# Kernel optimization log

Measured on AMD Instinct MI355X. Metric: run time of the kernel, lower is better.

Reference implementation:

```python
import jax, jax.numpy as jnp
import numpy as np

NUM_EMBEDDINGS = 4096
EMBEDDING_DIM = 512
N_TOKENS = 32768
COMMITMENT_COST = 0.25


def setup_inputs() -> dict:
    key = jax.random.key(0)
    k1, k2 = jax.random.split(key)
    flat_input = jax.random.normal(k1, (N_TOKENS, EMBEDDING_DIM), dtype=jnp.float32)
    # torch init: uniform(-1/K, 1/K)
    weight = jax.random.uniform(k2, (NUM_EMBEDDINGS, EMBEDDING_DIM), dtype=jnp.float32,
                                minval=-1.0 / NUM_EMBEDDINGS, maxval=1.0 / NUM_EMBEDDINGS)
    return {"flat_input": flat_input, "weight": weight}


def reference(flat_input, weight):
    distances = (jnp.sum(flat_input ** 2, axis=1, keepdims=True)
                 + jnp.sum(weight ** 2, axis=1)
                 - 2.0 * jnp.matmul(flat_input, weight.T))
    encoding_indices = jnp.argmin(distances, axis=1)  # [N]
    # one-hot @ weight == direct gather of codebook rows
    quantized = weight[encoding_indices]  # [N, D]

    e_latent_loss = jnp.mean((jax.lax.stop_gradient(quantized) - flat_input) ** 2, axis=1)
    q_latent_loss = jnp.mean((quantized - jax.lax.stop_gradient(flat_input)) ** 2, axis=1)
    loss = q_latent_loss + COMMITMENT_COST * e_latent_loss  # [N]

    # straight-through estimator
    quantized_st = flat_input + jax.lax.stop_gradient(quantized - flat_input)

    # avg_probs = mean of one-hot encodings over batch = normalized code counts
    counts = jnp.zeros((NUM_EMBEDDINGS,), dtype=flat_input.dtype).at[encoding_indices].add(1.0)
    avg_probs = counts / flat_input.shape[0]
    perplexity = jnp.exp(-jnp.sum(avg_probs * jnp.log(avg_probs + 1e-10)))

    return quantized_st, loss, perplexity, encoding_indices
```

## Files before the change

### kernel.cpp

```cpp
#include <hip/hip_runtime.h>
#include <math.h>

#define N_TOK 32768
#define K_CODES 4096
#define DIM 512
#define COMMIT 0.25f
#define NCAND 8
#define NSPLIT 2
#define SPLIT_CODES (K_CODES / NSPLIT)
#define NITER (SPLIT_CODES / 256)
#define BIAS 0.125f

typedef short s16x8 __attribute__((ext_vector_type(8)));
typedef float f32x4 __attribute__((ext_vector_type(4)));
typedef unsigned int uint32;
typedef unsigned long long u64;
typedef unsigned short u16;

__device__ __forceinline__ u16 f2bf(float f) {
    uint32 b = __float_as_uint(f);
    return (u16)((b + 0x7FFFu + ((b >> 16) & 1u)) >> 16);
}

__device__ __forceinline__ void gload16(const u16* g, u16* l) {
    __builtin_amdgcn_global_load_lds(
        (const __attribute__((address_space(1))) void*)g,
        (__attribute__((address_space(3))) void*)l,
        16, 0, 0);
}

__global__ __launch_bounds__(256) void tobf16_kernel(const float* __restrict__ src,
                                                     u16* __restrict__ dst, int n4) {
    int i = blockIdx.x * 256 + threadIdx.x;
    int stride = gridDim.x * 256;
    for (; i < n4; i += stride) {
        float4 v = ((const float4*)src)[i];
        ushort4 o;
        o.x = f2bf(v.x); o.y = f2bf(v.y); o.z = f2bf(v.z); o.w = f2bf(v.w);
        ((ushort4*)dst)[i] = o;
    }
}

__global__ __launch_bounds__(256) void rowsq_np_kernel(const float* __restrict__ a,
                                                       float* __restrict__ out,
                                                       int nrows) {
    #pragma clang fp contract(off)
    const int gw   = (blockIdx.x * 256 + threadIdx.x) >> 6;
    const int lane = threadIdx.x & 63;
    const int row  = gw * 8 + (lane >> 3);
    const int j    = lane & 7;
    if (row >= nrows) return;
    const float* p = a + (size_t)row * DIM;
    float blk[4];
    #pragma unroll
    for (int b = 0; b < 4; ++b) {
        const float* q = p + b * 128;
        float v = q[j];
        float r = v * v;
        for (int i = 8; i < 128; i += 8) { float u = q[i + j]; r += u * u; }
        float s1 = r  + __shfl_xor(r, 1);
        float s2 = s1 + __shfl_xor(s1, 2);
        float s3 = s2 + __shfl_xor(s2, 4);
        blk[b] = s3;
    }
    float res = (blk[0] + blk[1]) + (blk[2] + blk[3]);
    if (j == 0) out[row] = res;
}

__global__ __launch_bounds__(512, 2) void screen_kernel(const u16* __restrict__ xb,
                                                        const u16* __restrict__ wb,
                                                        const float* __restrict__ w2f,
                                                        u64* __restrict__ candPart) {
    __shared__ __attribute__((aligned(16))) u16 POOL[40960];

    const int tid  = threadIdx.x;
    const int wv   = tid >> 6;
    const int wt   = wv >> 2;
    const int wc   = wv & 3;
    const int lane = tid & 63;
    const int quad = lane >> 4;
    const int n15  = lane & 15;
    const int m0   = blockIdx.x * 64;
    const int sbase = blockIdx.y * SPLIT_CODES;

    const int l8  = lane >> 3;
    const int qsw = (lane & 7) ^ l8;

    const u16* xg0 = xb + (size_t)(m0 + wv * 8 + l8) * DIM + qsw * 8;
    const size_t wofs0 = (size_t)(wv * 32 + 0  + l8) * DIM;
    const size_t wofs1 = (size_t)(wv * 32 + 8  + l8) * DIM;
    const size_t wofs2 = (size_t)(wv * 32 + 16 + l8) * DIM;
    const size_t wofs3 = (size_t)(wv * 32 + 24 + l8) * DIM;

    u16* ldsx0 = &POOL[0    + wv * 512];
    u16* ldsx1 = &POOL[4096 + wv * 512];
    u16* ldsw0 = &POOL[8192  + wv * 2048];
    u16* ldsw1 = &POOL[24576 + wv * 2048];

    uint32 r1[8], r2[8];
    #pragma unroll
    for (int i = 0; i < 8; ++i) { r1[i] = 0xFFFFFFFFu; r2[i] = 0xFFFFFFFFu; }

    const u16* wit = wb + (size_t)sbase * DIM + qsw * 8;

    gload16(xg0, ldsx0);
    gload16(wit + wofs0, ldsw0);
    gload16(wit + wofs1, ldsw0 + 512);
    gload16(wit + wofs2, ldsw0 + 1024);
    gload16(wit + wofs3, ldsw0 + 1536);
    __syncthreads();

    for (int it = 0; it < NITER; ++it) {
        const int nbase = sbase + it * 256;

        float w2pb[4];
        #pragma unroll
        for (int c = 0; c < 4; ++c) w2pb[c] = w2f[nbase + wc * 64 + c * 16 + n15] + BIAS;

        f32x4 acc[2][4];
        #pragma unroll
        for (int i = 0; i < 2; ++i)
            #pragma unroll
            for (int c = 0; c < 4; ++c) acc[i][c] = (f32x4){0.f, 0.f, 0.f, 0.f};

        for (int kc = 0; kc < 8; ++kc) {
            if (kc < 7) {
                const int nb = (kc + 1) & 1;
                const int ko = (kc + 1) * 64;
                gload16(xg0 + ko, nb ? ldsx1 : ldsx0);
                u16* lw = nb ? ldsw1 : ldsw0;
                gload16(wit + wofs0 + ko, lw);
                gload16(wit + wofs1 + ko, lw + 512);
                gload16(wit + wofs2 + ko, lw + 1024);
                gload16(wit + wofs3 + ko, lw + 1536);
            } else if (it < NITER - 1) {
                const u16* wn = wit + (size_t)256 * DIM;
                gload16(xg0, ldsx0);
                gload16(wn + wofs0, ldsw0);
                gload16(wn + wofs1, ldsw0 + 512);
                gload16(wn + wofs2, ldsw0 + 1024);
                gload16(wn + wofs3, ldsw0 + 1536);
            }

            const u16* X = &POOL[(kc & 1) * 4096];
            const u16* W = &POOL[8192 + (kc & 1) * 16384];
            #pragma unroll
            for (int s = 0; s < 2; ++s) {
                const int lq = s * 4 + quad;
                s16x8 af[2], bf[4];
                #pragma unroll
                for (int i = 0; i < 2; ++i) {
                    const int tr = wt * 32 + i * 16 + n15;
                    af[i] = *(const s16x8*)&X[tr * 64 + (lq ^ (tr & 7)) * 8];
                }
                #pragma unroll
                for (int c = 0; c < 4; ++c) {
                    const int cr = wc * 64 + c * 16 + n15;
                    bf[c] = *(const s16x8*)&W[cr * 64 + (lq ^ (cr & 7)) * 8];
                }
                #pragma unroll
                for (int i = 0; i < 2; ++i)
                    #pragma unroll
                    for (int c = 0; c < 4; ++c)
                        acc[i][c] = __builtin_amdgcn_mfma_f32_16x16x32_bf16(af[i], bf[c], acc[i][c], 0, 0, 0);
            }
            __syncthreads();
        }

        #pragma unroll
        for (int i = 0; i < 2; ++i)
            #pragma unroll
            for (int r = 0; r < 4; ++r) {
                const int ti = i * 4 + r;
                #pragma unroll
                for (int c = 0; c < 4; ++c) {
                    float s = fmaf(-2.0f, acc[i][c][r], w2pb[c]);
                    uint32 key = (__float_as_uint(s) & 0xFFFFFFC0u) | (uint32)((it << 2) | c);
                    uint32 mx = r1[ti] > key ? r1[ti] : key;
                    r1[ti] = r1[ti] < key ? r1[ti] : key;
                    r2[ti] = r2[ti] < mx ? r2[ti] : mx;
                }
            }
        wit += (size_t)256 * DIM;
    }

    u64* MS = (u64*)POOL;
    #pragma unroll
    for (int ti = 0; ti < 8; ++ti) {
        const int i = ti >> 2, r = ti & 3;
        const int tloc = wt * 32 + i * 16 + quad * 4 + r;
        #pragma unroll
        for (int e = 0; e < 2; ++e) {
            uint32 k  = e ? r2[ti] : r1[ti];
            uint32 vb = k & 0xFFFFFFC0u;
            uint32 id = k & 63u;
            uint32 code = (uint32)(sbase + (id >> 2) * 256 + wc * 64 + (id & 3) * 16 + n15);
            MS[tloc * 128 + (wc * 16 + n15) * 2 + e] = ((u64)vb << 32) | code;
        }
    }
    __syncthreads();
    if (tid < 64) {
        u64 best[6];
        #pragma unroll
        for (int c = 0; c < 6; ++c) best[c] = 0xFFFFFFFFFFFFFFFFull;
        for (int e = 0; e < 128; ++e) {
            u64 v = MS[tid * 128 + e];
            if (v < best[5]) {
                best[5] = v;
                #pragma unroll
                for (int p = 5; p > 0; --p)
                    if (best[p] < best[p - 1]) { u64 tv = best[p]; best[p] = best[p - 1]; best[p - 1] = tv; }
            }
        }
        const int token = m0 + tid;
        u64* dst = candPart + ((size_t)blockIdx.y * N_TOK + token) * 6;
        #pragma unroll
        for (int c = 0; c < 6; ++c) dst[c] = best[c];
    }
}

__global__ __launch_bounds__(256) void mergecand_kernel(const u64* __restrict__ candPart,
                                                        int* __restrict__ candF) {
    int t = blockIdx.x * 256 + threadIdx.x;
    u64 best[NCAND];
    #pragma unroll
    for (int c = 0; c < NCAND; ++c) best[c] = 0xFFFFFFFFFFFFFFFFull;
    for (int s = 0; s < NSPLIT; ++s) {
        const u64* src = candPart + ((size_t)s * N_TOK + t) * 6;
        #pragma unroll
        for (int c = 0; c < 6; ++c) {
            u64 v = src[c];
            if (v < best[NCAND - 1]) {
                best[NCAND - 1] = v;
                #pragma unroll
                for (int p = NCAND - 1; p > 0; --p)
                    if (best[p] < best[p - 1]) { u64 tv = best[p]; best[p] = best[p - 1]; best[p - 1] = tv; }
            }
        }
    }
    #pragma unroll
    for (int c = 0; c < NCAND; ++c) candF[(size_t)t * NCAND + c] = (int)(best[c] & 0xFFFu);
}

__global__ __launch_bounds__(256) void refine_kernel(const float* __restrict__ x,
                                                     const float* __restrict__ w,
                                                     const float* __restrict__ x2np,
                                                     const float* __restrict__ w2np,
                                                     const int* __restrict__ cand,
                                                     int* __restrict__ idx) {
    const int t    = blockIdx.x * 4 + (threadIdx.x >> 6);
    const int lane = threadIdx.x & 63;

    const float* xr = x + (size_t)t * DIM;
    float xv[8];
    #pragma unroll
    for (int j = 0; j < 8; ++j) xv[j] = xr[lane + 64 * j];
    const float x2 = x2np[t];

    float bd = 3.4e38f;
    int   bk = 0x7fffffff;
    for (int c = 0; c < NCAND; ++c) {
        int k = cand[(size_t)t * NCAND + c];
        const float* wr = w + (size_t)k * DIM;
        double m = 0.0;
        #pragma unroll
        for (int j = 0; j < 8; ++j)
            m = fma((double)xv[j], (double)wr[lane + 64 * j], m);
        #pragma unroll
        for (int off = 32; off >= 1; off >>= 1) m += __shfl_down(m, off);
        if (lane == 0) {
            #pragma clang fp contract(off)
            float m32 = (float)m;
            float T1  = x2 + w2np[k];
            float d   = T1 - 2.0f * m32;
            if (d < bd || (d == bd && k < bk)) { bd = d; bk = k; }
        }
    }
    if (lane == 0) idx[t] = bk;
}

__global__ __launch_bounds__(256) void gather_kernel(const float* __restrict__ x,
                                                     const float* __restrict__ w,
                                                     const int* __restrict__ idx,
                                                     float* __restrict__ out_q,
                                                     float* __restrict__ out_loss,
                                                     float* __restrict__ out_ind,
                                                     int* __restrict__ counts) {
    const int wave = threadIdx.x >> 6;
    const int lane = threadIdx.x & 63;
    const int token = blockIdx.x * 4 + wave;
    const int k = idx[token];

    const float4* xr = (const float4*)(x + (size_t)token * DIM);
    const float4* wr = (const float4*)(w + (size_t)k * DIM);
    float4*       qo = (float4*)(out_q + (size_t)token * DIM);

    float ss = 0.f;
    #pragma unroll
    for (int j = 0; j < 2; ++j) {
        int e = lane + j * 64;
        float4 xv = xr[e];
        float4 wv = wr[e];
        float4 d, o;
        d.x = wv.x - xv.x; o.x = xv.x + d.x;
        d.y = wv.y - xv.y; o.y = xv.y + d.y;
        d.z = wv.z - xv.z; o.z = xv.z + d.z;
        d.w = wv.w - xv.w; o.w = xv.w + d.w;
        ss += d.x * d.x + d.y * d.y + d.z * d.z + d.w * d.w;
        qo[e] = o;
    }
    #pragma unroll
    for (int off = 32; off >= 1; off >>= 1) ss += __shfl_down(ss, off);
    if (lane == 0) {
        float lm = ss * (1.0f / DIM);
        out_loss[token] = lm + COMMIT * lm;
        out_ind[token] = (float)k;
        atomicAdd(&counts[k], 1);
    }
}

__global__ __launch_bounds__(256) void perplex_kernel(const int* __restrict__ counts,
                                                      float* __restrict__ out2) {
    __shared__ double red[4];
    const int tid = threadIdx.x;
    const int lane = tid & 63;
    const int wid = tid >> 6;
    double s = 0.0;
    for (int t = tid; t < K_CODES; t += 256) {
        int c = counts[t];
        if (c) {
            double p = (double)c * (1.0 / N_TOK);
            s += p * log(p + 1e-10);
        }
    }
    #pragma unroll
    for (int off = 32; off >= 1; off >>= 1) s += __shfl_down(s, off);
    if (lane == 0) red[wid] = s;
    __syncthreads();
    if (tid == 0) {
        double t = red[0] + red[1] + red[2] + red[3];
        out2[0] = (float)exp(-t);
    }
}

extern "C" void kernel_launch(void* const* d_in, const int* in_sizes, int n_in,
                              void* d_out, int out_size, void* d_ws, size_t ws_size,
                              hipStream_t stream) {
    const float* x = (const float*)d_in[0];
    const float* w = (const float*)d_in[1];

    float* out0 = (float*)d_out;
    float* out1 = out0 + (size_t)N_TOK * DIM;
    float* out2 = out1 + N_TOK;
    float* out3 = out2 + 1;

    u64*   candPart = (u64*)d_ws;
    float* x2np     = (float*)(candPart + (size_t)NSPLIT * N_TOK * 6);
    float* w2np     = x2np + N_TOK;
    int*   idx      = (int*)(w2np + K_CODES);
    int*   counts   = idx + N_TOK;
    int*   candF    = counts + K_CODES;
    u16*   x_bf     = (u16*)(candF + (size_t)N_TOK * NCAND);
    u16*   w_bf     = x_bf + (size_t)N_TOK * DIM;

    hipMemsetAsync(counts, 0, K_CODES * sizeof(int), stream);

    tobf16_kernel<<<4096, 256, 0, stream>>>(x, x_bf, N_TOK * DIM / 4);
    tobf16_kernel<<<2048, 256, 0, stream>>>(w, w_bf, K_CODES * DIM / 4);
    rowsq_np_kernel<<<N_TOK / 32, 256, 0, stream>>>(x, x2np, N_TOK);
    rowsq_np_kernel<<<K_CODES / 32, 256, 0, stream>>>(w, w2np, K_CODES);
    screen_kernel<<<dim3(N_TOK / 64, NSPLIT), 512, 0, stream>>>(x_bf, w_bf, w2np, candPart);
    mergecand_kernel<<<N_TOK / 256, 256, 0, stream>>>(candPart, candF);
    refine_kernel<<<N_TOK / 4, 256, 0, stream>>>(x, w, x2np, w2np, candF, idx);
    gather_kernel<<<N_TOK / 4, 256, 0, stream>>>(x, w, idx, out0, out1, out3, counts);
    perplex_kernel<<<1, 256, 0, stream>>>(counts, out2);
}
```

Measured before the change: 445.0 us.

## Triple-buffer LDS tiles with vmcnt-based waits in screen kernel

Replaces the double-buffered global-to-LDS pipeline with a three-stage ring buffer, prefetching two k-chunks ahead and waiting with explicit s_waitcnt vmcnt plus a raw barrier instead of a full __syncthreads after each chunk. It also hoists all per-iteration codebook norm loads into registers up front and fully unrolls the outer loop. The aim is to hide global load latency behind MFMA work. In exchange, LDS use per block rises (about 120KB), which may limit occupancy against the launch bound of 2 blocks, and the hoisted norms add register pressure.

```diff
diff --git a/kernel.cpp b/kernel.cpp
--- a/kernel.cpp
+++ b/kernel.cpp
@@ -71,7 +71,7 @@
                                                         const u16* __restrict__ wb,
                                                         const float* __restrict__ w2f,
                                                         u64* __restrict__ candPart) {
-    __shared__ __attribute__((aligned(16))) u16 POOL[40960];
+    __shared__ __attribute__((aligned(16))) u16 POOL[61440];
 
     const int tid  = threadIdx.x;
     const int wv   = tid >> 6;
@@ -86,37 +86,37 @@
     const int l8  = lane >> 3;
     const int qsw = (lane & 7) ^ l8;
 
-    const u16* xg0 = xb + (size_t)(m0 + wv * 8 + l8) * DIM + qsw * 8;
-    const size_t wofs0 = (size_t)(wv * 32 + 0  + l8) * DIM;
-    const size_t wofs1 = (size_t)(wv * 32 + 8  + l8) * DIM;
-    const size_t wofs2 = (size_t)(wv * 32 + 16 + l8) * DIM;
-    const size_t wofs3 = (size_t)(wv * 32 + 24 + l8) * DIM;
-
-    u16* ldsx0 = &POOL[0    + wv * 512];
-    u16* ldsx1 = &POOL[4096 + wv * 512];
-    u16* ldsw0 = &POOL[8192  + wv * 2048];
-    u16* ldsw1 = &POOL[24576 + wv * 2048];
+    const u16* xg = xb + (size_t)(m0 + wv * 8 + l8) * DIM + qsw * 8;
+    const u16* wg = wb + (size_t)(sbase + wv * 32 + l8) * DIM + qsw * 8;
+
+    const int xdst = wv * 512;
+    const int wdst = wv * 2048;
+
+    float w2all[NITER][4];
+    #pragma unroll
+    for (int it = 0; it < NITER; ++it)
+        #pragma unroll
+        for (int c = 0; c < 4; ++c)
+            w2all[it][c] = w2f[sbase + it * 256 + wc * 64 + c * 16 + n15] + BIAS;
 
     uint32 r1[8], r2[8];
     #pragma unroll
     for (int i = 0; i < 8; ++i) { r1[i] = 0xFFFFFFFFu; r2[i] = 0xFFFFFFFFu; }
 
-    const u16* wit = wb + (size_t)sbase * DIM + qsw * 8;
-
-    gload16(xg0, ldsx0);
-    gload16(wit + wofs0, ldsw0);
-    gload16(wit + wofs1, ldsw0 + 512);
-    gload16(wit + wofs2, ldsw0 + 1024);
-    gload16(wit + wofs3, ldsw0 + 1536);
+    #pragma unroll
+    for (int tt = 0; tt < 2; ++tt) {
+        gload16(xg + tt * 64, &POOL[tt * 4096 + xdst]);
+        #pragma unroll
+        for (int j = 0; j < 4; ++j)
+            gload16(wg + (size_t)(j * 8) * DIM + tt * 64,
+                    &POOL[12288 + tt * 16384 + wdst + j * 512]);
+    }
     __syncthreads();
 
+    int ic = 0, in_ = 1, ip = 2;
+
+    #pragma unroll
     for (int it = 0; it < NITER; ++it) {
-        const int nbase = sbase + it * 256;
-
-        float w2pb[4];
-        #pragma unroll
-        for (int c = 0; c < 4; ++c) w2pb[c] = w2f[nbase + wc * 64 + c * 16 + n15] + BIAS;
-
         f32x4 acc[2][4];
         #pragma unroll
         for (int i = 0; i < 2; ++i)
@@ -124,26 +124,14 @@
             for (int c = 0; c < 4; ++c) acc[i][c] = (f32x4){0.f, 0.f, 0.f, 0.f};
 
         for (int kc = 0; kc < 8; ++kc) {
-            if (kc < 7) {
-                const int nb = (kc + 1) & 1;
-                const int ko = (kc + 1) * 64;
-                gload16(xg0 + ko, nb ? ldsx1 : ldsx0);
-                u16* lw = nb ? ldsw1 : ldsw0;
-                gload16(wit + wofs0 + ko, lw);
-                gload16(wit + wofs1 + ko, lw + 512);
-                gload16(wit + wofs2 + ko, lw + 1024);
-                gload16(wit + wofs3 + ko, lw + 1536);
-            } else if (it < NITER - 1) {
-                const u16* wn = wit + (size_t)256 * DIM;
-                gload16(xg0, ldsx0);
-                gload16(wn + wofs0, ldsw0);
-                gload16(wn + wofs1, ldsw0 + 512);
-                gload16(wn + wofs2, ldsw0 + 1024);
-                gload16(wn + wofs3, ldsw0 + 1536);
-            }
-
-            const u16* X = &POOL[(kc & 1) * 4096];
-            const u16* W = &POOL[8192 + (kc & 1) * 16384];
+            const int t = it * 8 + kc;
+            if (t < 63) asm volatile("s_waitcnt vmcnt(5)" ::: "memory");
+            else        asm volatile("s_waitcnt vmcnt(0)" ::: "memory");
+            __builtin_amdgcn_s_barrier();
+            __builtin_amdgcn_sched_barrier(0);
+
+            const u16* X = &POOL[ic * 4096];
+            const u16* W = &POOL[12288 + ic * 16384];
             #pragma unroll
             for (int s = 0; s < 2; ++s) {
                 const int lq = s * 4 + quad;
@@ -164,7 +152,18 @@
                     for (int c = 0; c < 4; ++c)
                         acc[i][c] = __builtin_amdgcn_mfma_f32_16x16x32_bf16(af[i], bf[c], acc[i][c], 0, 0, 0);
             }
-            __syncthreads();
+
+            if (t <= 61) {
+                const int kcu = (kc + 2) & 7;
+                const int itu = it + ((kc + 2) >> 3);
+                gload16(xg + kcu * 64, &POOL[ip * 4096 + xdst]);
+                const u16* wsrc = wg + (size_t)itu * (256 * DIM) + kcu * 64;
+                #pragma unroll
+                for (int j = 0; j < 4; ++j)
+                    gload16(wsrc + (size_t)(j * 8) * DIM,
+                            &POOL[12288 + ip * 16384 + wdst + j * 512]);
+            }
+            int tmp = ic; ic = in_; in_ = ip; ip = tmp;
         }
 
         #pragma unroll
@@ -174,16 +173,16 @@
                 const int ti = i * 4 + r;
                 #pragma unroll
                 for (int c = 0; c < 4; ++c) {
-                    float s = fmaf(-2.0f, acc[i][c][r], w2pb[c]);
+                    float s = fmaf(-2.0f, acc[i][c][r], w2all[it][c]);
                     uint32 key = (__float_as_uint(s) & 0xFFFFFFC0u) | (uint32)((it << 2) | c);
                     uint32 mx = r1[ti] > key ? r1[ti] : key;
                     r1[ti] = r1[ti] < key ? r1[ti] : key;
                     r2[ti] = r2[ti] < mx ? r2[ti] : mx;
                 }
             }
-        wit += (size_t)256 * DIM;
-    }
-
+    }
+
+    __syncthreads();
     u64* MS = (u64*)POOL;
     #pragma unroll
     for (int ti = 0; ti < 8; ++ti) {
```

Measured after the change: 473.5 us. 1.06x slower.
